# Optimization experiments

Measured on AMD Instinct MI355X. Metric: run time of the kernel, lower is better.

## Reference

```python
import jax, jax.numpy as jnp
import numpy as np

N_NODES = 100000
N_EDGES = 1600000
NEG_SLOPE = 0.01  # F.leaky_relu default


def _param(key, shape, scale=0.05):
    return jax.random.normal(key, shape, dtype=jnp.float32) * scale


def setup_inputs() -> dict:
    key = jax.random.key(0)
    ks = jax.random.split(key, 32)
    inp = {
        "x": jax.random.normal(ks[0], (N_NODES, 64), dtype=jnp.float32),
        "edge_index": jax.random.randint(ks[1], (2, N_EDGES), 0, N_NODES, dtype=jnp.int64),
        # encoder SAGEConv params: lin_l (neighbors, with bias) + lin_r (root)
        "ggn1_Wl": _param(ks[2], (128, 64)), "ggn1_b": jnp.zeros((128,), jnp.float32), "ggn1_Wr": _param(ks[3], (128, 64)),
        "ggn2_Wl": _param(ks[4], (128, 128)), "ggn2_b": jnp.zeros((128,), jnp.float32), "ggn2_Wr": _param(ks[5], (128, 128)),
        "ggn3_Wl": _param(ks[6], (128, 128)), "ggn3_b": jnp.zeros((128,), jnp.float32), "ggn3_Wr": _param(ks[7], (128, 128)),
        "tr2_W": _param(ks[8], (64, 128)), "tr2_b": jnp.zeros((64,), jnp.float32),
        # decoder
        "dec1_W": _param(ks[9], (128, 64)), "dec1_b": jnp.zeros((128,), jnp.float32),
        "dec2_Wl": _param(ks[10], (128, 128)), "dec2_b": jnp.zeros((128,), jnp.float32), "dec2_Wr": _param(ks[11], (128, 128)),
        "dec3_Wl": _param(ks[12], (64, 128)), "dec3_b": jnp.zeros((64,), jnp.float32), "dec3_Wr": _param(ks[13], (64, 128)),
        "dec4_Wl": _param(ks[14], (3, 64)), "dec4_b": jnp.zeros((3,), jnp.float32), "dec4_Wr": _param(ks[15], (3, 64)),
    }
    return inp


def _sage(x, src, dst, Wl, b, Wr, n):
    # PyG SAGEConv (aggr='mean'): lin_l(mean_{j->i} x_j) + lin_r(x_i)
    msgs = x[src]                                              # [E, d] gather
    s = jax.ops.segment_sum(msgs, dst, num_segments=n)          # [N, d]
    cnt = jax.ops.segment_sum(jnp.ones((src.shape[0], 1), x.dtype), dst, num_segments=n)
    mean = s / jnp.maximum(cnt, 1.0)
    return mean @ Wl.T + b + x @ Wr.T


def _leaky(h):
    return jnp.where(h > 0, h, NEG_SLOPE * h)


def reference(x, edge_index,
              ggn1_Wl, ggn1_b, ggn1_Wr,
              ggn2_Wl, ggn2_b, ggn2_Wr,
              ggn3_Wl, ggn3_b, ggn3_Wr,
              tr2_W, tr2_b,
              dec1_W, dec1_b,
              dec2_Wl, dec2_b, dec2_Wr,
              dec3_Wl, dec3_b, dec3_Wr,
              dec4_Wl, dec4_b, dec4_Wr):
    n = x.shape[0]
    src, dst = edge_index[0], edge_index[1]  # source_to_target flow
    # --- encode (dropout = identity, deterministic reference) ---
    h = jnp.tanh(_sage(x, src, dst, ggn1_Wl, ggn1_b, ggn1_Wr, n))
    h = jnp.tanh(_sage(h, src, dst, ggn2_Wl, ggn2_b, ggn2_Wr, n))
    h = jnp.tanh(_sage(h, src, dst, ggn3_Wl, ggn3_b, ggn3_Wr, n))
    mu = h @ tr2_W.T + tr2_b
    logvar = mu  # module applies the same tr2 twice
    z = mu       # reparametrize in eval mode returns mu
    # --- decode ---
    o = _leaky(z @ dec1_W.T + dec1_b)
    o = _leaky(_sage(o, src, dst, dec2_Wl, dec2_b, dec2_Wr, n))
    o = jnp.tanh(_sage(o, src, dst, dec3_Wl, dec3_b, dec3_Wr, n))
    z2 = _sage(o, src, dst, dec4_Wl, dec4_b, dec4_Wr, n)
    return (z2[:, :2], z2[:, 2], mu, logvar)
```

## Files before the change

kernel.cpp:

```cpp
#include <hip/hip_runtime.h>
#include <cmath>


constexpr int ACT_NONE = 0, ACT_TANH = 1, ACT_LEAKY = 2;
constexpr int SCAN_CHUNK = 4096;

typedef __attribute__((ext_vector_type(8))) __bf16 bf16x8;
typedef __attribute__((ext_vector_type(4))) float f32x4;
typedef __attribute__((ext_vector_type(4))) unsigned short u16x4;
typedef __attribute__((ext_vector_type(8))) unsigned short u16x8;

__device__ __forceinline__ unsigned short f2h(float x) {
  _Float16 h = (_Float16)x;
  unsigned short u;
  __builtin_memcpy(&u, &h, 2);
  return u;
}
__device__ __forceinline__ float hlo(unsigned int u) {
  unsigned short s = (unsigned short)(u & 0xffffu);
  _Float16 h;
  __builtin_memcpy(&h, &s, 2);
  return (float)h;
}
__device__ __forceinline__ float hhi(unsigned int u) {
  unsigned short s = (unsigned short)(u >> 16);
  _Float16 h;
  __builtin_memcpy(&h, &s, 2);
  return (float)h;
}
__device__ __forceinline__ void split_bf16(float x, __bf16& h, __bf16& l) {
  h = (__bf16)x;
  l = (__bf16)(x - (float)h);
}
__device__ __forceinline__ unsigned short b2u(__bf16 b) {
  unsigned short u;
  __builtin_memcpy(&u, &b, 2);
  return u;
}

__global__ __launch_bounds__(256) void split_x_kernel(const float* __restrict__ in,
                                                      __bf16* __restrict__ hi,
                                                      __bf16* __restrict__ lo, int total) {
  int i = (blockIdx.x * 256 + threadIdx.x) * 4;
  if (i >= total) return;
  float4 v = *(const float4*)(in + i);
  float vv[4] = {v.x, v.y, v.z, v.w};
  u16x4 h, l;
#pragma unroll
  for (int j = 0; j < 4; ++j) {
    __bf16 hb, lb;
    split_bf16(vv[j], hb, lb);
    h[j] = b2u(hb);
    l[j] = b2u(lb);
  }
  *(u16x4*)(hi + i) = h;
  *(u16x4*)(lo + i) = l;
}

__global__ __launch_bounds__(256) void split_w_kernel(
    const float* p0, const float* p1, const float* p2, const float* p3,
    const float* p4, const float* p5, const float* p6, const float* p7,
    const float* p8, const float* p9, const float* p10, const float* p11,
    __bf16* __restrict__ hi, __bf16* __restrict__ lo) {
  int b = blockIdx.x;
  const float* src;
  int boff, doff;
  if      (b < 8)   { src = p0;  boff = b;       doff = 0; }
  else if (b < 16)  { src = p1;  boff = b - 8;   doff = 8192; }
  else if (b < 32)  { src = p2;  boff = b - 16;  doff = 16384; }
  else if (b < 48)  { src = p3;  boff = b - 32;  doff = 32768; }
  else if (b < 64)  { src = p4;  boff = b - 48;  doff = 49152; }
  else if (b < 80)  { src = p5;  boff = b - 64;  doff = 65536; }
  else if (b < 88)  { src = p6;  boff = b - 80;  doff = 81920; }
  else if (b < 96)  { src = p7;  boff = b - 88;  doff = 90112; }
  else if (b < 112) { src = p8;  boff = b - 96;  doff = 98304; }
  else if (b < 128) { src = p9;  boff = b - 112; doff = 114688; }
  else if (b < 136) { src = p10; boff = b - 128; doff = 131072; }
  else              { src = p11; boff = b - 136; doff = 139264; }
  int i = boff * 1024 + threadIdx.x * 4;
  float4 v = *(const float4*)(src + i);
  float vv[4] = {v.x, v.y, v.z, v.w};
  u16x4 h, l;
#pragma unroll
  for (int j = 0; j < 4; ++j) {
    __bf16 hb, lb;
    split_bf16(vv[j], hb, lb);
    h[j] = b2u(hb);
    l[j] = b2u(lb);
  }
  *(u16x4*)(hi + doff + i) = h;
  *(u16x4*)(lo + doff + i) = l;
}

__global__ __launch_bounds__(256) void count_rank_kernel(const int* __restrict__ dst,
                                                         int* __restrict__ cnt,
                                                         int* __restrict__ rank, int E) {
  int e = blockIdx.x * 256 + threadIdx.x;
  if (e < E) rank[e] = atomicAdd(&cnt[dst[e]], 1);
}

__global__ __launch_bounds__(1024) void scan_blk_kernel(const int* __restrict__ cnt,
                                                        int* __restrict__ rowptr,
                                                        float* __restrict__ inv,
                                                        int* __restrict__ bsum, int n) {
  __shared__ int wsum[17];
  const int lane = threadIdx.x & 63;
  const int wid = threadIdx.x >> 6;
  const int i0 = blockIdx.x * SCAN_CHUNK + threadIdx.x * 4;
  int v[4];
  if (i0 + 3 < n) {
    int4 t = *(const int4*)(cnt + i0);
    v[0] = t.x; v[1] = t.y; v[2] = t.z; v[3] = t.w;
  } else {
#pragma unroll
    for (int j = 0; j < 4; ++j) v[j] = (i0 + j < n) ? cnt[i0 + j] : 0;
  }
#pragma unroll
  for (int j = 0; j < 4; ++j)
    if (i0 + j < n) inv[i0 + j] = 1.0f / (float)(v[j] > 1 ? v[j] : 1);
  const int s = v[0] + v[1] + v[2] + v[3];
  int x = s;
#pragma unroll
  for (int off = 1; off < 64; off <<= 1) {
    int t = __shfl_up(x, off);
    if (lane >= off) x += t;
  }
  if (lane == 63) wsum[wid + 1] = x;
  __syncthreads();
  if (threadIdx.x == 0) {
    wsum[0] = 0;
    for (int w = 1; w <= 16; ++w) wsum[w] += wsum[w - 1];
    bsum[blockIdx.x] = wsum[16];
  }
  __syncthreads();
  int p = wsum[wid] + x - s;
#pragma unroll
  for (int j = 0; j < 4; ++j) {
    if (i0 + j < n) rowptr[i0 + j] = p;
    p += v[j];
  }
}

__global__ __launch_bounds__(1024) void scan_sums_kernel(int* __restrict__ bsum,
                                                         int* __restrict__ rowptr,
                                                         int nb, int n) {
  __shared__ int wsum[17];
  const int lane = threadIdx.x & 63;
  const int wid = threadIdx.x >> 6;
  const int v = (threadIdx.x < nb) ? bsum[threadIdx.x] : 0;
  int x = v;
#pragma unroll
  for (int off = 1; off < 64; off <<= 1) {
    int t = __shfl_up(x, off);
    if (lane >= off) x += t;
  }
  if (lane == 63) wsum[wid + 1] = x;
  __syncthreads();
  if (threadIdx.x == 0) {
    wsum[0] = 0;
    for (int w = 1; w <= 16; ++w) wsum[w] += wsum[w - 1];
    rowptr[n] = wsum[16];
  }
  __syncthreads();
  if (threadIdx.x < nb) bsum[threadIdx.x] = wsum[wid] + x - v;
}

__global__ __launch_bounds__(1024) void scan_add_kernel(int* __restrict__ rowptr,
                                                        const int* __restrict__ bsum,
                                                        int n) {
  const int off = bsum[blockIdx.x];
  const int i0 = blockIdx.x * SCAN_CHUNK + threadIdx.x * 4;
  if (i0 + 3 < n) {
    int4 t = *(const int4*)(rowptr + i0);
    t.x += off; t.y += off; t.z += off; t.w += off;
    *(int4*)(rowptr + i0) = t;
  } else {
    for (int j = 0; j < 4; ++j)
      if (i0 + j < n) rowptr[i0 + j] += off;
  }
}

__global__ __launch_bounds__(256) void scatter_kernel(const int* __restrict__ src,
                                                      const int* __restrict__ dst,
                                                      const int* __restrict__ rowptr,
                                                      const int* __restrict__ rank,
                                                      int* __restrict__ esrc, int E) {
  int e = blockIdx.x * 256 + threadIdx.x;
  if (e < E) esrc[rowptr[dst[e]] + rank[e]] = src[e];
}

__global__ __launch_bounds__(256) void gather_f32s_kernel(
    const float* __restrict__ in, const int* __restrict__ esrc,
    const int* __restrict__ rowptr, const float* __restrict__ inv,
    __bf16* __restrict__ Mhi, __bf16* __restrict__ Mlo, int n) {
  const int node = blockIdx.x * 4 + (threadIdx.x >> 6);
  const int lane = threadIdx.x & 63;
  if (node >= n) return;
  const int beg = rowptr[node];
  const int end = rowptr[node + 1];
  const float iv = inv[node];
  float a0 = 0.f, a1 = 0.f, a2 = 0.f, a3 = 0.f;
  for (int b = beg; b < end; b += 64) {
    int m = end - b;
    if (m > 64) m = 64;
    int myi = (lane < m) ? esrc[b + lane] : 0;
    int s = 0;
    for (; s + 4 <= m; s += 4) {
      int i0 = __shfl(myi, s);
      int i1 = __shfl(myi, s + 1);
      int i2 = __shfl(myi, s + 2);
      int i3 = __shfl(myi, s + 3);
      a0 += in[(size_t)i0 * 64 + lane];
      a1 += in[(size_t)i1 * 64 + lane];
      a2 += in[(size_t)i2 * 64 + lane];
      a3 += in[(size_t)i3 * 64 + lane];
    }
    for (; s < m; ++s) {
      int i0 = __shfl(myi, s);
      a0 += in[(size_t)i0 * 64 + lane];
    }
  }
  float mv = ((a0 + a1) + (a2 + a3)) * iv;
  __bf16 h, l;
  split_bf16(mv, h, l);
  Mhi[(size_t)node * 64 + lane] = h;
  Mlo[(size_t)node * 64 + lane] = l;
}

__global__ __launch_bounds__(256) void gather_s16_kernel(
    const unsigned short* __restrict__ inq, const int* __restrict__ esrc,
    const int* __restrict__ rowptr, const float* __restrict__ inv,
    __bf16* __restrict__ Mhi, __bf16* __restrict__ Mlo, int n) {
  const int node = blockIdx.x * 4 + (threadIdx.x >> 6);
  const int lane = threadIdx.x & 63;
  if (node >= n) return;
  const int beg = rowptr[node];
  const int end = rowptr[node + 1];
  const float iv = inv[node] * (1.0f / 32767.0f);
  const unsigned int* bu = (const unsigned int*)inq;
  int a0l = 0, a0h = 0, a1l = 0, a1h = 0;
  int a2l = 0, a2h = 0, a3l = 0, a3h = 0;
  for (int b = beg; b < end; b += 64) {
    int m = end - b;
    if (m > 64) m = 64;
    int myi = (lane < m) ? esrc[b + lane] : 0;
    int s = 0;
    for (; s + 4 <= m; s += 4) {
      int i0 = __shfl(myi, s);
      int i1 = __shfl(myi, s + 1);
      int i2 = __shfl(myi, s + 2);
      int i3 = __shfl(myi, s + 3);
      unsigned int u0 = bu[(size_t)i0 * 64 + lane];
      unsigned int u1 = bu[(size_t)i1 * 64 + lane];
      unsigned int u2 = bu[(size_t)i2 * 64 + lane];
      unsigned int u3 = bu[(size_t)i3 * 64 + lane];
      a0l += (int)(short)u0; a0h += ((int)u0) >> 16;
      a1l += (int)(short)u1; a1h += ((int)u1) >> 16;
      a2l += (int)(short)u2; a2h += ((int)u2) >> 16;
      a3l += (int)(short)u3; a3h += ((int)u3) >> 16;
    }
    for (; s < m; ++s) {
      int i0 = __shfl(myi, s);
      unsigned int u0 = bu[(size_t)i0 * 64 + lane];
      a0l += (int)(short)u0; a0h += ((int)u0) >> 16;
    }
  }
  float rx = (float)((a0l + a1l) + (a2l + a3l)) * iv;
  float ry = (float)((a0h + a1h) + (a2h + a3h)) * iv;
  __bf16 h0, l0, h1, l1;
  split_bf16(rx, h0, l0);
  split_bf16(ry, h1, l1);
  ((unsigned int*)Mhi)[(size_t)node * 64 + lane] =
      (unsigned int)b2u(h0) | ((unsigned int)b2u(h1) << 16);
  ((unsigned int*)Mlo)[(size_t)node * 64 + lane] =
      (unsigned int)b2u(l0) | ((unsigned int)b2u(l1) << 16);
}

__global__ __launch_bounds__(256) void gather_h128_kernel(
    const unsigned short* __restrict__ inh, const int* __restrict__ esrc,
    const int* __restrict__ rowptr, const float* __restrict__ inv,
    __bf16* __restrict__ Mhi, __bf16* __restrict__ Mlo, int n) {
  const int node = blockIdx.x * 4 + (threadIdx.x >> 6);
  const int lane = threadIdx.x & 63;
  if (node >= n) return;
  const int beg = rowptr[node];
  const int end = rowptr[node + 1];
  const float iv = inv[node];
  const unsigned int* bu = (const unsigned int*)inh;
  float a0x = 0.f, a0y = 0.f, a1x = 0.f, a1y = 0.f;
  float a2x = 0.f, a2y = 0.f, a3x = 0.f, a3y = 0.f;
  for (int b = beg; b < end; b += 64) {
    int m = end - b;
    if (m > 64) m = 64;
    int myi = (lane < m) ? esrc[b + lane] : 0;
    int s = 0;
    for (; s + 4 <= m; s += 4) {
      int i0 = __shfl(myi, s);
      int i1 = __shfl(myi, s + 1);
      int i2 = __shfl(myi, s + 2);
      int i3 = __shfl(myi, s + 3);
      unsigned int u0 = bu[(size_t)i0 * 64 + lane];
      unsigned int u1 = bu[(size_t)i1 * 64 + lane];
      unsigned int u2 = bu[(size_t)i2 * 64 + lane];
      unsigned int u3 = bu[(size_t)i3 * 64 + lane];
      a0x += hlo(u0); a0y += hhi(u0);
      a1x += hlo(u1); a1y += hhi(u1);
      a2x += hlo(u2); a2y += hhi(u2);
      a3x += hlo(u3); a3y += hhi(u3);
    }
    for (; s < m; ++s) {
      int i0 = __shfl(myi, s);
      unsigned int u0 = bu[(size_t)i0 * 64 + lane];
      a0x += hlo(u0); a0y += hhi(u0);
    }
  }
  float rx = ((a0x + a1x) + (a2x + a3x)) * iv;
  float ry = ((a0y + a1y) + (a2y + a3y)) * iv;
  __bf16 h0, l0, h1, l1;
  split_bf16(rx, h0, l0);
  split_bf16(ry, h1, l1);
  ((unsigned int*)Mhi)[(size_t)node * 64 + lane] =
      (unsigned int)b2u(h0) | ((unsigned int)b2u(h1) << 16);
  ((unsigned int*)Mlo)[(size_t)node * 64 + lane] =
      (unsigned int)b2u(l0) | ((unsigned int)b2u(l1) << 16);
}

__global__ __launch_bounds__(256) void gather_h64_kernel(
    const unsigned short* __restrict__ inh, const int* __restrict__ esrc,
    const int* __restrict__ rowptr, const float* __restrict__ inv,
    float* __restrict__ meanb, int n) {
  const int node = blockIdx.x * 4 + (threadIdx.x >> 6);
  const int lane = threadIdx.x & 63;
  if (node >= n) return;
  const int beg = rowptr[node];
  const int end = rowptr[node + 1];
  const float iv = inv[node];
  const unsigned int* bu = (const unsigned int*)inh;
  const int half = lane >> 5;
  const int hl = lane & 31;
  float ax = 0.f, ay = 0.f, bx = 0.f, by = 0.f;
  for (int b = beg; b < end; b += 64) {
    int m = end - b;
    if (m > 64) m = 64;
    int myi = (lane < m) ? esrc[b + lane] : 0;
    int s = 0;
    for (; s + 4 <= m; s += 4) {
      int i0 = __shfl(myi, s + half);
      int i1 = __shfl(myi, s + 2 + half);
      unsigned int u0 = bu[(size_t)i0 * 32 + hl];
      unsigned int u1 = bu[(size_t)i1 * 32 + hl];
      ax += hlo(u0); ay += hhi(u0);
      bx += hlo(u1); by += hhi(u1);
    }
    for (; s < m; s += 2) {
      int t = s + half;
      if (t < m) {
        int i0 = __shfl(myi, t);
        unsigned int u0 = bu[(size_t)i0 * 32 + hl];
        ax += hlo(u0); ay += hhi(u0);
      }
    }
  }
  float sx = ax + bx, sy = ay + by;
  sx += __shfl_xor(sx, 32);
  sy += __shfl_xor(sy, 32);
  if (half == 0)
    ((float2*)meanb)[(size_t)node * 32 + hl] = make_float2(sx * iv, sy * iv);
}

__global__ __launch_bounds__(256) void gather_mean4_kernel(
    const float* __restrict__ y4, const int* __restrict__ esrc,
    const int* __restrict__ rowptr, const float* __restrict__ inv,
    float* __restrict__ mean4, int n) {
  int i = blockIdx.x * 256 + threadIdx.x;
  if (i >= n) return;
  const int beg = rowptr[i], end = rowptr[i + 1];
  const float iv = inv[i];
  float sx = 0.f, sy = 0.f, sz = 0.f;
  const float4* b = (const float4*)y4;
  for (int j = beg; j < end; ++j) {
    float4 v = b[esrc[j]];
    sx += v.x; sy += v.y; sz += v.z;
  }
  ((float4*)mean4)[i] = make_float4(sx * iv, sy * iv, sz * iv, 0.f);
}

template <int DI, int DO, int ACT, bool AGG, bool ADDMEAN, bool BIAS, int SH,
          bool OSPLIT, int ASRC>
__global__ __launch_bounds__(512) void node_mfma_kernel(
    const __bf16* __restrict__ Ahi, const __bf16* __restrict__ Alo,
    const __bf16* __restrict__ Mhi, const __bf16* __restrict__ Mlo,
    const __bf16* __restrict__ Wrhi, const __bf16* __restrict__ Wrlo,
    const __bf16* __restrict__ Wlhi, const __bf16* __restrict__ Wllo,
    const float* __restrict__ bias, const float* __restrict__ meanF,
    float* __restrict__ out, float* __restrict__ out2,
    unsigned short* __restrict__ outh,
    __bf16* __restrict__ ohi, __bf16* __restrict__ olo, int n) {
  constexpr int BM = 256;
  constexpr int KSW = DI + 8;
  constexpr int CT = DO / 16;
  constexpr int EL = DO * DI / 512;
  __shared__ __align__(16) __bf16 Ws_hi[DO * KSW];
  __shared__ __align__(16) __bf16 Ws_lo[DO * KSW];

  const int wv = threadIdx.x >> 6;
  const int lane = threadIdx.x & 63;
  const int lm = lane & 15;
  const int lq = lane >> 4;
  const int row0 = blockIdx.x * BM;

  f32x4 acc[2][CT];
#pragma unroll
  for (int rt = 0; rt < 2; ++rt)
#pragma unroll
    for (int ct = 0; ct < CT; ++ct) acc[rt][ct] = (f32x4){0.f, 0.f, 0.f, 0.f};

  bf16x8 zf;
#pragma unroll
  for (int j = 0; j < 8; ++j) zf[j] = (__bf16)0.f;

  const int rA0 = row0 + wv * 32 + lm;
  const int rA1 = rA0 + 16;
  const bool ok0 = rA0 < n;
  const bool ok1 = rA1 < n;
  const int kofs = lq * 8;

  const int sc = (threadIdx.x * EL) / DI;
  const int sk = (threadIdx.x * EL) % DI;

  const int nphase = AGG ? 2 : 1;
  for (int phase = 0; phase < nphase; ++phase) {
    const __bf16* WH = (phase == 0) ? Wrhi : Wlhi;
    const __bf16* WL = (phase == 0) ? Wrlo : Wllo;
    if (phase > 0) __syncthreads();
#pragma unroll
    for (int j = 0; j < EL / 8; ++j) {
      *(bf16x8*)(&Ws_hi[sc * KSW + sk + j * 8]) =
          *(const bf16x8*)(WH + (size_t)sc * DI + sk + j * 8);
      *(bf16x8*)(&Ws_lo[sc * KSW + sk + j * 8]) =
          *(const bf16x8*)(WL + (size_t)sc * DI + sk + j * 8);
    }
    __syncthreads();

    const __bf16* AH = (phase == 0) ? Ahi : Mhi;
    const __bf16* AL = (phase == 0) ? Alo : Mlo;
#pragma unroll
    for (int k0 = 0; k0 < DI; k0 += 32) {
      bf16x8 ah[2], al[2];
      if (ASRC == 2 && phase == 0) {
        const unsigned short* Q = (const unsigned short*)AH;
        u16x8 q0, q1;
        if (ok0) q0 = *(const u16x8*)(Q + (size_t)rA0 * DI + k0 + kofs);
        else {
#pragma unroll
          for (int j = 0; j < 8; ++j) q0[j] = 0;
        }
        if (ok1) q1 = *(const u16x8*)(Q + (size_t)rA1 * DI + k0 + kofs);
        else {
#pragma unroll
          for (int j = 0; j < 8; ++j) q1[j] = 0;
        }
#pragma unroll
        for (int j = 0; j < 8; ++j) {
          __bf16 hb, lb;
          split_bf16((float)(short)q0[j] * (1.0f / 32767.0f), hb, lb);
          ah[0][j] = hb; al[0][j] = lb;
          split_bf16((float)(short)q1[j] * (1.0f / 32767.0f), hb, lb);
          ah[1][j] = hb; al[1][j] = lb;
        }
      } else {
        ah[0] = ok0 ? *(const bf16x8*)(AH + (size_t)rA0 * DI + k0 + kofs) : zf;
        al[0] = ok0 ? *(const bf16x8*)(AL + (size_t)rA0 * DI + k0 + kofs) : zf;
        ah[1] = ok1 ? *(const bf16x8*)(AH + (size_t)rA1 * DI + k0 + kofs) : zf;
        al[1] = ok1 ? *(const bf16x8*)(AL + (size_t)rA1 * DI + k0 + kofs) : zf;
      }
#pragma unroll
      for (int ct = 0; ct < CT; ++ct) {
        const int c = ct * 16 + lm;
        bf16x8 bh = *(const bf16x8*)(&Ws_hi[c * KSW + k0 + kofs]);
        bf16x8 bl = *(const bf16x8*)(&Ws_lo[c * KSW + k0 + kofs]);
#pragma unroll
        for (int rt = 0; rt < 2; ++rt) {
          acc[rt][ct] = __builtin_amdgcn_mfma_f32_16x16x32_bf16(ah[rt], bh, acc[rt][ct], 0, 0, 0);
          acc[rt][ct] = __builtin_amdgcn_mfma_f32_16x16x32_bf16(al[rt], bh, acc[rt][ct], 0, 0, 0);
          acc[rt][ct] = __builtin_amdgcn_mfma_f32_16x16x32_bf16(ah[rt], bl, acc[rt][ct], 0, 0, 0);
        }
      }
    }
  }

#pragma unroll
  for (int rt = 0; rt < 2; ++rt)
#pragma unroll
    for (int ct = 0; ct < CT; ++ct) {
      const int col = ct * 16 + lm;
      const float bval = BIAS ? bias[col] : 0.f;
      f32x4 a = acc[rt][ct];
#pragma unroll
      for (int r = 0; r < 4; ++r) {
        const int row = row0 + wv * 32 + rt * 16 + lq * 4 + r;
        if (row < n) {
          float t = a[r] + bval;
          if (ADDMEAN) t += meanF[(size_t)row * DO + col];
          if (ACT == ACT_TANH) t = tanhf(t);
          else if (ACT == ACT_LEAKY) t = (t > 0.f) ? t : 0.01f * t;
          if (out) out[(size_t)row * DO + col] = t;
          if (out2) out2[(size_t)row * DO + col] = t;
          if constexpr (SH == 1) {
            if (outh) outh[(size_t)row * DO + col] = f2h(t);
          } else if constexpr (SH == 2) {
            if (outh)
              outh[(size_t)row * DO + col] =
                  (unsigned short)(short)__builtin_rintf(t * 32767.0f);
          }
          if constexpr (OSPLIT) {
            __bf16 hb, lb;
            split_bf16(t, hb, lb);
            ohi[(size_t)row * DO + col] = hb;
            olo[(size_t)row * DO + col] = lb;
          }
        }
      }
    }
}

__global__ __launch_bounds__(256) void dec4_pre_kernel(
    const float* __restrict__ hB, const float* __restrict__ Wl,
    float* __restrict__ y4, int n) {
  const int node = blockIdx.x * 4 + (threadIdx.x >> 6);
  const int lane = threadIdx.x & 63;
  if (node >= n) return;
  float v = hB[(size_t)node * 64 + lane];
  float p0 = v * Wl[lane];
  float p1 = v * Wl[64 + lane];
  float p2 = v * Wl[128 + lane];
#pragma unroll
  for (int off = 32; off >= 1; off >>= 1) {
    p0 += __shfl_xor(p0, off);
    p1 += __shfl_xor(p1, off);
    p2 += __shfl_xor(p2, off);
  }
  if (lane == 0) ((float4*)y4)[node] = make_float4(p0, p1, p2, 0.f);
}

__global__ __launch_bounds__(256) void dec4_final_kernel(
    const float* __restrict__ hB, const float* __restrict__ mean4,
    const float* __restrict__ Wr, const float* __restrict__ bias,
    float* __restrict__ out, int n) {
  const int node = blockIdx.x * 4 + (threadIdx.x >> 6);
  const int lane = threadIdx.x & 63;
  if (node >= n) return;
  float v = hB[(size_t)node * 64 + lane];
  float p0 = v * Wr[lane];
  float p1 = v * Wr[64 + lane];
  float p2 = v * Wr[128 + lane];
#pragma unroll
  for (int off = 32; off >= 1; off >>= 1) {
    p0 += __shfl_xor(p0, off);
    p1 += __shfl_xor(p1, off);
    p2 += __shfl_xor(p2, off);
  }
  if (lane == 0) {
    float4 m = ((const float4*)mean4)[node];
    out[2 * (size_t)node]     = p0 + m.x + bias[0];
    out[2 * (size_t)node + 1] = p1 + m.y + bias[1];
    out[2 * (size_t)n + node] = p2 + m.z + bias[2];
  }
}

extern "C" void kernel_launch(void* const* d_in, const int* in_sizes, int n_in,
                              void* d_out, int out_size, void* d_ws, size_t ws_size,
                              hipStream_t stream) {
  const float* x = (const float*)d_in[0];
  const int* ei = (const int*)d_in[1];
  const int N = in_sizes[0] / 64;
  const int E = in_sizes[1] / 2;
  const int* src = ei;
  const int* dst = ei + E;
  const float* g1Wl = (const float*)d_in[2];
  const float* g1b  = (const float*)d_in[3];
  const float* g1Wr = (const float*)d_in[4];
  const float* g2Wl = (const float*)d_in[5];
  const float* g2b  = (const float*)d_in[6];
  const float* g2Wr = (const float*)d_in[7];
  const float* g3Wl = (const float*)d_in[8];
  const float* g3b  = (const float*)d_in[9];
  const float* g3Wr = (const float*)d_in[10];
  const float* t2W  = (const float*)d_in[11];
  const float* t2b  = (const float*)d_in[12];
  const float* d1W  = (const float*)d_in[13];
  const float* d1b  = (const float*)d_in[14];
  const float* d2Wl = (const float*)d_in[15];
  const float* d2b  = (const float*)d_in[16];
  const float* d2Wr = (const float*)d_in[17];
  const float* d3Wl = (const float*)d_in[18];
  const float* d3b  = (const float*)d_in[19];
  const float* d3Wr = (const float*)d_in[20];
  const float* d4Wl = (const float*)d_in[21];
  const float* d4b  = (const float*)d_in[22];
  const float* d4Wr = (const float*)d_in[23];

  const size_t N64 = (size_t)N * 64;
  const size_t N128 = (size_t)N * 128;

  char* w = (char*)d_ws;
  auto alloc = [&](size_t bytes) {
    char* p = w;
    w += (bytes + 255) & ~(size_t)255;
    return p;
  };
  __bf16* Ahi = (__bf16*)alloc(N128 * 2);
  __bf16* Alo = (__bf16*)alloc(N128 * 2);
  __bf16* Bhi = (__bf16*)alloc(N128 * 2);
  __bf16* Blo = (__bf16*)alloc(N128 * 2);
  float*  meanF = (float*)alloc(N128 * 4);
  __bf16* xhi = (__bf16*)alloc(N64 * 2);
  __bf16* xlo = (__bf16*)alloc(N64 * 2);
  __bf16* Whi = (__bf16*)alloc(147456 * 2);
  __bf16* Wlo = (__bf16*)alloc(147456 * 2);
  int*    cnt = (int*)alloc((size_t)N * 4);
  float*  inv = (float*)alloc((size_t)N * 4);
  int*    rowp = (int*)alloc(((size_t)N + 1) * 4);
  int*    rank = (int*)alloc((size_t)E * 4);
  int*    esrc = (int*)alloc((size_t)E * 4);
  unsigned short* shB = (unsigned short*)alloc(N128 * 2);

  unsigned short* act1 = (unsigned short*)Ahi;
  unsigned short* act2 = (unsigned short*)Alo;

  __bf16* Mhi = (__bf16*)meanF;
  __bf16* Mlo = Mhi + N128;
  int*    bsum = (int*)meanF;
  float*  y4 = meanF;
  float*  mean4 = meanF + 4 * (size_t)N;
  float*  hBf = meanF + N64;
  __bf16* muhi = xhi;
  __bf16* mulo = xlo;
  unsigned short* shC = (unsigned short*)xhi;

  float* out = (float*)d_out;
  float* mu  = out + 3 * (size_t)N;
  float* lv  = mu + 64 * (size_t)N;

  const int NB = (N + 255) / 256;
  const int GB = (N + 3) / 4;
  const int SB = (N + SCAN_CHUNK - 1) / SCAN_CHUNK;

  const __bf16 *W_g1Wl_h = Whi + 0,      *W_g1Wl_l = Wlo + 0;
  const __bf16 *W_g1Wr_h = Whi + 8192,   *W_g1Wr_l = Wlo + 8192;
  const __bf16 *W_g2Wl_h = Whi + 16384,  *W_g2Wl_l = Wlo + 16384;
  const __bf16 *W_g2Wr_h = Whi + 32768,  *W_g2Wr_l = Wlo + 32768;
  const __bf16 *W_g3Wl_h = Whi + 49152,  *W_g3Wl_l = Wlo + 49152;
  const __bf16 *W_g3Wr_h = Whi + 65536,  *W_g3Wr_l = Wlo + 65536;
  const __bf16 *W_t2W_h  = Whi + 81920,  *W_t2W_l  = Wlo + 81920;
  const __bf16 *W_d1W_h  = Whi + 90112,  *W_d1W_l  = Wlo + 90112;
  const __bf16 *W_d2Wl_h = Whi + 98304,  *W_d2Wl_l = Wlo + 98304;
  const __bf16 *W_d2Wr_h = Whi + 114688, *W_d2Wr_l = Wlo + 114688;
  const __bf16 *W_d3Wl_h = Whi + 131072, *W_d3Wl_l = Wlo + 131072;
  const __bf16 *W_d3Wr_h = Whi + 139264, *W_d3Wr_l = Wlo + 139264;

  split_x_kernel<<<(int)((N64 + 1023) / 1024), 256, 0, stream>>>(x, xhi, xlo, (int)N64);
  split_w_kernel<<<144, 256, 0, stream>>>(g1Wl, g1Wr, g2Wl, g2Wr, g3Wl, g3Wr,
                                          t2W, d1W, d2Wl, d2Wr, d3Wl, d3Wr, Whi, Wlo);

  hipMemsetAsync(cnt, 0, (size_t)N * sizeof(int), stream);
  count_rank_kernel<<<(E + 255) / 256, 256, 0, stream>>>(dst, cnt, rank, E);
  scan_blk_kernel<<<SB, 1024, 0, stream>>>(cnt, rowp, inv, bsum, N);
  scan_sums_kernel<<<1, 1024, 0, stream>>>(bsum, rowp, SB, N);
  scan_add_kernel<<<SB, 1024, 0, stream>>>(rowp, bsum, N);
  scatter_kernel<<<(E + 255) / 256, 256, 0, stream>>>(src, dst, rowp, rank, esrc, E);

  gather_f32s_kernel<<<GB, 256, 0, stream>>>(x, esrc, rowp, inv, Mhi, Mlo, N);
  node_mfma_kernel<64, 128, ACT_TANH, true, false, true, 2, false, 0><<<NB, 512, 0, stream>>>(
      xhi, xlo, Mhi, Mlo, W_g1Wr_h, W_g1Wr_l, W_g1Wl_h, W_g1Wl_l, g1b, nullptr,
      nullptr, nullptr, act1, nullptr, nullptr, N);

  gather_s16_kernel<<<GB, 256, 0, stream>>>(act1, esrc, rowp, inv, Mhi, Mlo, N);
  node_mfma_kernel<128, 128, ACT_TANH, true, false, true, 2, false, 2><<<NB, 512, 0, stream>>>(
      (const __bf16*)act1, nullptr, Mhi, Mlo, W_g2Wr_h, W_g2Wr_l, W_g2Wl_h, W_g2Wl_l,
      g2b, nullptr, nullptr, nullptr, act2, nullptr, nullptr, N);

  gather_s16_kernel<<<GB, 256, 0, stream>>>(act2, esrc, rowp, inv, Mhi, Mlo, N);
  node_mfma_kernel<128, 128, ACT_TANH, true, false, true, 2, false, 2><<<NB, 512, 0, stream>>>(
      (const __bf16*)act2, nullptr, Mhi, Mlo, W_g3Wr_h, W_g3Wr_l, W_g3Wl_h, W_g3Wl_l,
      g3b, nullptr, nullptr, nullptr, act1, nullptr, nullptr, N);

  node_mfma_kernel<128, 64, ACT_NONE, false, false, true, 0, true, 2><<<NB, 512, 0, stream>>>(
      (const __bf16*)act1, nullptr, nullptr, nullptr, W_t2W_h, W_t2W_l, nullptr, nullptr,
      t2b, nullptr, mu, lv, nullptr, muhi, mulo, N);

  node_mfma_kernel<64, 128, ACT_LEAKY, false, false, true, 1, true, 0><<<NB, 512, 0, stream>>>(
      muhi, mulo, nullptr, nullptr, W_d1W_h, W_d1W_l, nullptr, nullptr, d1b, nullptr,
      nullptr, nullptr, shB, Bhi, Blo, N);

  gather_h128_kernel<<<GB, 256, 0, stream>>>(shB, esrc, rowp, inv, Mhi, Mlo, N);
  node_mfma_kernel<128, 128, ACT_LEAKY, true, false, true, 0, true, 0><<<NB, 512, 0, stream>>>(
      Bhi, Blo, Mhi, Mlo, W_d2Wr_h, W_d2Wr_l, W_d2Wl_h, W_d2Wl_l, d2b, nullptr,
      nullptr, nullptr, nullptr, Ahi, Alo, N);

  node_mfma_kernel<128, 64, ACT_NONE, false, false, false, 1, false, 0><<<NB, 512, 0, stream>>>(
      Ahi, Alo, nullptr, nullptr, W_d3Wl_h, W_d3Wl_l, nullptr, nullptr, nullptr, nullptr,
      nullptr, nullptr, shC, nullptr, nullptr, N);
  gather_h64_kernel<<<GB, 256, 0, stream>>>(shC, esrc, rowp, inv, meanF, N);
  node_mfma_kernel<128, 64, ACT_TANH, false, true, true, 0, false, 0><<<NB, 512, 0, stream>>>(
      Ahi, Alo, nullptr, nullptr, W_d3Wr_h, W_d3Wr_l, nullptr, nullptr, d3b, meanF,
      hBf, nullptr, nullptr, nullptr, nullptr, N);

  dec4_pre_kernel<<<GB, 256, 0, stream>>>(hBf, d4Wl, y4, N);
  gather_mean4_kernel<<<(N + 255) / 256, 256, 0, stream>>>(y4, esrc, rowp, inv, mean4, N);
  dec4_final_kernel<<<GB, 256, 0, stream>>>(hBf, mean4, d4Wr, d4b, out, N);
}
```

Before: 894.3 us.

## Build CSR via two-level bucketed counting sort with shared-memory histograms

Replaces the global-atomic count/rank plus random scatter CSR construction with a two-pass bucket sort. Edges are first binned by dst>>8 using per-chunk shared-memory histograms, then the histograms are scanned. Edges are placed into buckets as packed (src,dst) pairs, and each bucket is finished locally with a shared-memory count, scan and placement. This avoids contended global atomics and scattered writes, at the cost of an extra 8-byte-per-edge temporary pass and a nondeterministic ordering of edges within a node.

```diff
diff --git a/kernel.cpp b/kernel.cpp
--- a/kernel.cpp
+++ b/kernel.cpp
@@ -4,6 +4,8 @@
 
 constexpr int ACT_NONE = 0, ACT_TANH = 1, ACT_LEAKY = 2;
 constexpr int SCAN_CHUNK = 4096;
+constexpr int CSR_CHUNK = 4096;
+constexpr int MAXB = 512;
 
 typedef __attribute__((ext_vector_type(8))) __bf16 bf16x8;
 typedef __attribute__((ext_vector_type(4))) float f32x4;
@@ -92,15 +94,24 @@
   *(u16x4*)(lo + doff + i) = l;
 }
 
-__global__ __launch_bounds__(256) void count_rank_kernel(const int* __restrict__ dst,
-                                                         int* __restrict__ cnt,
-                                                         int* __restrict__ rank, int E) {
-  int e = blockIdx.x * 256 + threadIdx.x;
-  if (e < E) rank[e] = atomicAdd(&cnt[dst[e]], 1);
+__global__ __launch_bounds__(256) void csr_hist_kernel(const int* __restrict__ dst,
+                                                       int* __restrict__ histT,
+                                                       int C, int NBK, int E) {
+  __shared__ int lh[MAXB];
+  const int c = blockIdx.x;
+  for (int b = threadIdx.x; b < NBK; b += 256) lh[b] = 0;
+  __syncthreads();
+  const int base = c * CSR_CHUNK;
+  for (int k = 0; k < CSR_CHUNK; k += 256) {
+    int e = base + k + threadIdx.x;
+    if (e < E) atomicAdd(&lh[dst[e] >> 8], 1);
+  }
+  __syncthreads();
+  for (int b = threadIdx.x; b < NBK; b += 256) histT[b * C + c] = lh[b];
 }
 
 __global__ __launch_bounds__(1024) void scan_blk_kernel(const int* __restrict__ cnt,
-                                                        int* __restrict__ rowptr,
+                                                        int* __restrict__ outp,
                                                         float* __restrict__ inv,
                                                         int* __restrict__ bsum, int n) {
   __shared__ int wsum[17];
@@ -115,9 +126,11 @@
 #pragma unroll
     for (int j = 0; j < 4; ++j) v[j] = (i0 + j < n) ? cnt[i0 + j] : 0;
   }
-#pragma unroll
-  for (int j = 0; j < 4; ++j)
-    if (i0 + j < n) inv[i0 + j] = 1.0f / (float)(v[j] > 1 ? v[j] : 1);
+  if (inv) {
+#pragma unroll
+    for (int j = 0; j < 4; ++j)
+      if (i0 + j < n) inv[i0 + j] = 1.0f / (float)(v[j] > 1 ? v[j] : 1);
+  }
   const int s = v[0] + v[1] + v[2] + v[3];
   int x = s;
 #pragma unroll
@@ -136,13 +149,13 @@
   int p = wsum[wid] + x - s;
 #pragma unroll
   for (int j = 0; j < 4; ++j) {
-    if (i0 + j < n) rowptr[i0 + j] = p;
+    if (i0 + j < n) outp[i0 + j] = p;
     p += v[j];
   }
 }
 
 __global__ __launch_bounds__(1024) void scan_sums_kernel(int* __restrict__ bsum,
-                                                         int* __restrict__ rowptr,
+                                                         int* __restrict__ outp,
                                                          int nb, int n) {
   __shared__ int wsum[17];
   const int lane = threadIdx.x & 63;
@@ -159,34 +172,92 @@
   if (threadIdx.x == 0) {
     wsum[0] = 0;
     for (int w = 1; w <= 16; ++w) wsum[w] += wsum[w - 1];
-    rowptr[n] = wsum[16];
+    outp[n] = wsum[16];
   }
   __syncthreads();
   if (threadIdx.x < nb) bsum[threadIdx.x] = wsum[wid] + x - v;
 }
 
-__global__ __launch_bounds__(1024) void scan_add_kernel(int* __restrict__ rowptr,
+__global__ __launch_bounds__(1024) void scan_add_kernel(int* __restrict__ outp,
                                                         const int* __restrict__ bsum,
                                                         int n) {
   const int off = bsum[blockIdx.x];
   const int i0 = blockIdx.x * SCAN_CHUNK + threadIdx.x * 4;
   if (i0 + 3 < n) {
-    int4 t = *(const int4*)(rowptr + i0);
+    int4 t = *(const int4*)(outp + i0);
     t.x += off; t.y += off; t.z += off; t.w += off;
-    *(int4*)(rowptr + i0) = t;
+    *(int4*)(outp + i0) = t;
   } else {
     for (int j = 0; j < 4; ++j)
-      if (i0 + j < n) rowptr[i0 + j] += off;
-  }
-}
-
-__global__ __launch_bounds__(256) void scatter_kernel(const int* __restrict__ src,
-                                                      const int* __restrict__ dst,
-                                                      const int* __restrict__ rowptr,
-                                                      const int* __restrict__ rank,
-                                                      int* __restrict__ esrc, int E) {
-  int e = blockIdx.x * 256 + threadIdx.x;
-  if (e < E) esrc[rowptr[dst[e]] + rank[e]] = src[e];
+      if (i0 + j < n) outp[i0 + j] += off;
+  }
+}
+
+__global__ __launch_bounds__(256) void csr_place_kernel(
+    const int* __restrict__ src, const int* __restrict__ dst,
+    const int* __restrict__ histS, unsigned long long* __restrict__ tmp,
+    int C, int NBK, int E) {
+  __shared__ int lc[MAXB];
+  const int c = blockIdx.x;
+  for (int b = threadIdx.x; b < NBK; b += 256) lc[b] = histS[b * C + c];
+  __syncthreads();
+  const int base = c * CSR_CHUNK;
+  for (int k = 0; k < CSR_CHUNK; k += 256) {
+    int e = base + k + threadIdx.x;
+    if (e < E) {
+      int d = dst[e];
+      int pos = atomicAdd(&lc[d >> 8], 1);
+      tmp[pos] = ((unsigned long long)(unsigned)src[e] << 32) | (unsigned)d;
+    }
+  }
+}
+
+__global__ __launch_bounds__(256) void csr_final_kernel(
+    const unsigned long long* __restrict__ tmp, const int* __restrict__ histS,
+    int* __restrict__ rowptr, float* __restrict__ inv, int* __restrict__ esrc,
+    int C, int n, int E) {
+  __shared__ int lcnt[256];
+  __shared__ int lptr[256];
+  __shared__ int wsum[5];
+  const int b = blockIdx.x;
+  const int S = histS[b * C];
+  const int Eb = histS[(b + 1) * C];
+  lcnt[threadIdx.x] = 0;
+  __syncthreads();
+  for (int j = S + threadIdx.x; j < Eb; j += 256)
+    atomicAdd(&lcnt[(int)(tmp[j] & 255u)], 1);
+  __syncthreads();
+  const int lane = threadIdx.x & 63;
+  const int wid = threadIdx.x >> 6;
+  const int v = lcnt[threadIdx.x];
+  int x = v;
+#pragma unroll
+  for (int off = 1; off < 64; off <<= 1) {
+    int t = __shfl_up(x, off);
+    if (lane >= off) x += t;
+  }
+  if (lane == 63) wsum[wid + 1] = x;
+  __syncthreads();
+  if (threadIdx.x == 0) {
+    wsum[0] = 0;
+    for (int w = 1; w <= 3; ++w) wsum[w] += wsum[w - 1];
+  }
+  __syncthreads();
+  const int ex = wsum[wid] + x - v;
+  lptr[threadIdx.x] = ex;
+  const int node = b * 256 + threadIdx.x;
+  if (node < n) {
+    rowptr[node] = S + ex;
+    inv[node] = 1.0f / (float)(v > 1 ? v : 1);
+  }
+  if (b == 0 && threadIdx.x == 0) rowptr[n] = E;
+  __syncthreads();
+  for (int j = S + threadIdx.x; j < Eb; j += 256) {
+    unsigned long long t = tmp[j];
+    int ln = (int)(t & 255u);
+    int pos = S + atomicAdd(&lptr[ln], 1);
+    esrc[pos] = (int)(t >> 32);
+  }
 }
 
 __global__ __launch_bounds__(256) void gather_f32s_kernel(
@@ -603,6 +674,10 @@
   const size_t N64 = (size_t)N * 64;
   const size_t N128 = (size_t)N * 128;
 
+  const int NBK = (N + 255) / 256;
+  const int C = (E + CSR_CHUNK - 1) / CSR_CHUNK;
+  const int L = NBK * C;
+
   char* w = (char*)d_ws;
   auto alloc = [&](size_t bytes) {
     char* p = w;
@@ -618,11 +693,12 @@
   __bf16* xlo = (__bf16*)alloc(N64 * 2);
   __bf16* Whi = (__bf16*)alloc(147456 * 2);
   __bf16* Wlo = (__bf16*)alloc(147456 * 2);
-  int*    cnt = (int*)alloc((size_t)N * 4);
   float*  inv = (float*)alloc((size_t)N * 4);
   int*    rowp = (int*)alloc(((size_t)N + 1) * 4);
-  int*    rank = (int*)alloc((size_t)E * 4);
+  unsigned long long* tmp = (unsigned long long*)alloc((size_t)E * 8);
   int*    esrc = (int*)alloc((size_t)E * 4);
+  int*    histT = (int*)alloc((size_t)L * 4);
+  int*    histS = (int*)alloc(((size_t)L + 1) * 4);
   unsigned short* shB = (unsigned short*)alloc(N128 * 2);
 
   unsigned short* act1 = (unsigned short*)Ahi;
@@ -644,7 +720,7 @@
 
   const int NB = (N + 255) / 256;
   const int GB = (N + 3) / 4;
-  const int SB = (N + SCAN_CHUNK - 1) / SCAN_CHUNK;
+  const int SB2 = (L + SCAN_CHUNK - 1) / SCAN_CHUNK;
 
   const __bf16 *W_g1Wl_h = Whi + 0,      *W_g1Wl_l = Wlo + 0;
   const __bf16 *W_g1Wr_h = Whi + 8192,   *W_g1Wr_l = Wlo + 8192;
@@ -663,12 +739,12 @@
   split_w_kernel<<<144, 256, 0, stream>>>(g1Wl, g1Wr, g2Wl, g2Wr, g3Wl, g3Wr,
                                           t2W, d1W, d2Wl, d2Wr, d3Wl, d3Wr, Whi, Wlo);
 
-  hipMemsetAsync(cnt, 0, (size_t)N * sizeof(int), stream);
-  count_rank_kernel<<<(E + 255) / 256, 256, 0, stream>>>(dst, cnt, rank, E);
-  scan_blk_kernel<<<SB, 1024, 0, stream>>>(cnt, rowp, inv, bsum, N);
-  scan_sums_kernel<<<1, 1024, 0, stream>>>(bsum, rowp, SB, N);
-  scan_add_kernel<<<SB, 1024, 0, stream>>>(rowp, bsum, N);
-  scatter_kernel<<<(E + 255) / 256, 256, 0, stream>>>(src, dst, rowp, rank, esrc, E);
+  csr_hist_kernel<<<C, 256, 0, stream>>>(dst, histT, C, NBK, E);
+  scan_blk_kernel<<<SB2, 1024, 0, stream>>>(histT, histS, nullptr, bsum, L);
+  scan_sums_kernel<<<1, 1024, 0, stream>>>(bsum, histS, SB2, L);
+  scan_add_kernel<<<SB2, 1024, 0, stream>>>(histS, bsum, L);
+  csr_place_kernel<<<C, 256, 0, stream>>>(src, dst, histS, tmp, C, NBK, E);
+  csr_final_kernel<<<NBK, 256, 0, stream>>>(tmp, histS, rowp, inv, esrc, C, N, E);
 
   gather_f32s_kernel<<<GB, 256, 0, stream>>>(x, esrc, rowp, inv, Mhi, Mlo, N);
   node_mfma_kernel<64, 128, ACT_TANH, true, false, true, 2, false, 0><<<NB, 512, 0, stream>>>(
```

Result: slower. 1.001 ms (+11.9%).
